# Kernel optimization log

Measured on AMD Instinct MI355X. Metric: run time of the kernel, lower is better.

## Reference

```python
import jax, jax.numpy as jnp
import numpy as np

L, H, NH, NKV, HD, FF, V = 2, 2048, 16, 2, 128, 11008, 32000
B, S, R, LORA_SCALE = 32, 64, 16, 2.0  # lora scaling = alpha/r = 32/16
PH, TD = 1024, 512
ROPE_THETA = 1e6

def _rms(x, w, eps=1e-6):
    return x * jax.lax.rsqrt(jnp.mean(x * x, axis=-1, keepdims=True) + eps) * w

def _rot_half(x):
    h = x.shape[-1] // 2
    return jnp.concatenate([-x[..., h:], x[..., :h]], axis=-1)

def _lora_linear(x, W, A, Bm, b=None):
    y = x @ W.T + LORA_SCALE * ((x @ A.T) @ Bm.T)
    return y + b if b is not None else y

def _forward(input_ids, attention_mask, embed, Wq, bq, Aq, Bq, Wk, bk, Ak, Bk,
             Wv, bv, Av, Bv, Wo, Ao, Bo, ln1, ln2, Wg, Wu, Wd, norm_f,
             W1, b1, W2, b2):
    Bsz, Sl = input_ids.shape
    h = embed[input_ids]                                            # [B,S,H]
    inv_freq = 1.0 / (ROPE_THETA ** (jnp.arange(0, HD, 2, dtype=jnp.float32) / HD))
    ang = jnp.arange(Sl, dtype=jnp.float32)[:, None] * inv_freq      # [S,HD/2]
    cos = jnp.concatenate([jnp.cos(ang)] * 2, -1)[None, :, None, :]  # [1,S,1,HD]
    sin = jnp.concatenate([jnp.sin(ang)] * 2, -1)[None, :, None, :]
    causal = jnp.tril(jnp.ones((Sl, Sl), dtype=bool))
    keep = causal[None, None] & (attention_mask[:, None, None, :] > 0)
    bias = jnp.where(keep, 0.0, -1e9).astype(jnp.float32)            # [B,1,S,S]
    for l in range(L):
        x = _rms(h, ln1[l])
        q = _lora_linear(x, Wq[l], Aq[l], Bq[l], bq[l]).reshape(Bsz, Sl, NH, HD)
        k = _lora_linear(x, Wk[l], Ak[l], Bk[l], bk[l]).reshape(Bsz, Sl, NKV, HD)
        v = _lora_linear(x, Wv[l], Av[l], Bv[l], bv[l]).reshape(Bsz, Sl, NKV, HD)
        q = q * cos + _rot_half(q) * sin
        k = k * cos + _rot_half(k) * sin
        k = jnp.repeat(k, NH // NKV, axis=2)                         # GQA expand
        v = jnp.repeat(v, NH // NKV, axis=2)
        scores = jnp.einsum('bqhd,bkhd->bhqk', q, k) / np.sqrt(HD).astype(np.float32) + bias
        p = jax.nn.softmax(scores, axis=-1)
        attn = jnp.einsum('bhqk,bkhd->bqhd', p, v).reshape(Bsz, Sl, H)
        h = h + _lora_linear(attn, Wo[l], Ao[l], Bo[l])
        x = _rms(h, ln2[l])
        h = h + (jax.nn.silu(x @ Wg[l].T) * (x @ Wu[l].T)) @ Wd[l].T  # SwiGLU MLP
    h = _rms(h, norm_f)                       # final norm -> hidden_states[-1]
    seq_len = jnp.sum(attention_mask, axis=1) - 1
    pooled = h[jnp.arange(Bsz), seq_len]      # last valid token  [B,H]
    z = jax.nn.gelu(pooled @ W1.T + b1, approximate=False)
    return (z @ W2.T + b2).astype(jnp.float32)  # [B,512]

def setup_inputs():
    key = jax.random.key(0)
    ks = jax.random.split(key, 32)
    def n(k, shape, s=0.02):
        return (s * jax.random.normal(k, shape)).astype(jnp.float32)
    lens = jax.random.randint(ks[0], (B,), 1, S + 1)
    return {
        'input_ids': jax.random.randint(ks[1], (B, S), 0, V, dtype=jnp.int32),
        'attention_mask': (jnp.arange(S)[None, :] < lens[:, None]).astype(jnp.int32),
        'embed': n(ks[2], (V, H)),
        'Wq': n(ks[3], (L, H, H)), 'bq': n(ks[4], (L, H)),
        'Aq': n(ks[5], (L, R, H)), 'Bq': n(ks[6], (L, H, R)),
        'Wk': n(ks[7], (L, NKV * HD, H)), 'bk': n(ks[8], (L, NKV * HD)),
        'Ak': n(ks[9], (L, R, H)), 'Bk': n(ks[10], (L, NKV * HD, R)),
        'Wv': n(ks[11], (L, NKV * HD, H)), 'bv': n(ks[12], (L, NKV * HD)),
        'Av': n(ks[13], (L, R, H)), 'Bv': n(ks[14], (L, NKV * HD, R)),
        'Wo': n(ks[15], (L, H, H)),
        'Ao': n(ks[16], (L, R, H)), 'Bo': n(ks[17], (L, H, R)),
        'ln1': jnp.ones((L, H), jnp.float32), 'ln2': jnp.ones((L, H), jnp.float32),
        'Wg': n(ks[18], (L, FF, H)), 'Wu': n(ks[19], (L, FF, H)), 'Wd': n(ks[20], (L, H, FF)),
        'norm_f': jnp.ones((H,), jnp.float32),
        'W1': n(ks[21], (PH, H)), 'b1': jnp.zeros((PH,), jnp.float32),
        'W2': n(ks[22], (TD, PH)), 'b2': jnp.zeros((TD,), jnp.float32),
    }

def reference(input_ids, attention_mask, embed, Wq, bq, Aq, Bq, Wk, bk, Ak, Bk,
              Wv, bv, Av, Bv, Wo, Ao, Bo, ln1, ln2, Wg, Wu, Wd, norm_f,
              W1, b1, W2, b2):
    return _forward(input_ids, attention_mask, embed, Wq, bq, Aq, Bq, Wk, bk, Ak, Bk,
                    Wv, bv, Av, Bv, Wo, Ao, Bo, ln1, ln2, Wg, Wu, Wd, norm_f,
                    W1, b1, W2, b2)
```

## Files before the change

kernel.cpp:

```cpp
#include <hip/hip_runtime.h>
#include <hip/hip_bf16.h>
#include <math.h>

namespace {
constexpr int NL  = 2;
constexpr int H   = 2048;
constexpr int NH  = 16;
constexpr int NKV = 2;
constexpr int HD  = 128;
constexpr int FF  = 11008;
constexpr int BB  = 32;
constexpr int SS  = 64;
constexpr int RR  = 16;
constexpr int TT  = BB * SS;
constexpr int KVD = NKV * HD;
constexpr int QKVD = H + 2 * KVD;
constexpr int PH  = 1024, TDm = 512;
constexpr float LSCALE = 2.0f;
}

typedef __bf16 bf16x8 __attribute__((ext_vector_type(8)));
typedef float  f32x4  __attribute__((ext_vector_type(4)));

__device__ __forceinline__ ushort4 f4_to_bf4(float4 r) {
  __hip_bfloat16 a = __float2bfloat16(r.x), b = __float2bfloat16(r.y),
                 c = __float2bfloat16(r.z), d = __float2bfloat16(r.w);
  return make_ushort4(*(unsigned short*)&a, *(unsigned short*)&b,
                      *(unsigned short*)&c, *(unsigned short*)&d);
}

__device__ __forceinline__ bf16x8 f8cvt(float4 a, float4 b) {
  bf16x8 r;
  r[0] = (__bf16)a.x; r[1] = (__bf16)a.y; r[2] = (__bf16)a.z; r[3] = (__bf16)a.w;
  r[4] = (__bf16)b.x; r[5] = (__bf16)b.y; r[6] = (__bf16)b.z; r[7] = (__bf16)b.w;
  return r;
}

__device__ __forceinline__ float dot4(float4 a, float4 b) {
  return a.x * b.x + a.y * b.y + a.z * b.z + a.w * b.w;
}

__global__ __launch_bounds__(256) void k_embed(const int* __restrict__ ids,
                                               const float* __restrict__ emb,
                                               float* __restrict__ h) {
  int t = blockIdx.x;
  long id = ids[t];
  const float4* src = reinterpret_cast<const float4*>(emb + id * (long)H);
  float4* dst = reinterpret_cast<float4*>(h + (long)t * H);
  for (int i = threadIdx.x; i < H / 4; i += 256) dst[i] = src[i];
}

__global__ __launch_bounds__(256) void k_cvt(const float* __restrict__ src,
                                             __hip_bfloat16* __restrict__ dst, long n) {
  long i = ((long)blockIdx.x * 256 + threadIdx.x) * 4;
  if (i >= n) return;
  float4 v = *reinterpret_cast<const float4*>(src + i);
  *reinterpret_cast<ushort4*>(dst + i) = f4_to_bf4(v);
}

__global__ __launch_bounds__(256) void k_cvt_qkv(
    const float* __restrict__ Wq, const float* __restrict__ Wk,
    const float* __restrict__ Wv, __hip_bfloat16* __restrict__ dst) {
  long i = ((long)blockIdx.x * 256 + threadIdx.x) * 4;
  const long n1 = (long)H * H, n2 = n1 + (long)KVD * H, nt = (long)QKVD * H;
  if (i >= nt) return;
  const float* src; long off;
  if (i < n1)      { src = Wq; off = i; }
  else if (i < n2) { src = Wk; off = i - n1; }
  else             { src = Wv; off = i - n2; }
  float4 v = *reinterpret_cast<const float4*>(src + off);
  *reinterpret_cast<ushort4*>(dst + i) = f4_to_bf4(v);
}

__global__ __launch_bounds__(256) void k_cvt3(
    const float* __restrict__ s0, const float* __restrict__ s1,
    const float* __restrict__ s2, __hip_bfloat16* __restrict__ dst) {
  long i = ((long)blockIdx.x * 256 + threadIdx.x) * 4;
  const long n = (long)FF * H;
  if (i >= 3 * n) return;
  const float* src; long off;
  if (i < n)          { src = s0; off = i; }
  else if (i < 2 * n) { src = s1; off = i - n; }
  else                { src = s2; off = i - 2 * n; }
  float4 v = *reinterpret_cast<const float4*>(src + off);
  *reinterpret_cast<ushort4*>(dst + i) = f4_to_bf4(v);
}

__global__ __launch_bounds__(256) void k_prep(
    const float* __restrict__ bq, const float* __restrict__ bk, const float* __restrict__ bv,
    const float* __restrict__ Bq, const float* __restrict__ Bk, const float* __restrict__ Bv,
    float* __restrict__ biascat, float* __restrict__ bcat) {
  int idx = blockIdx.x * 256 + threadIdx.x;
  if (idx >= NL * QKVD) return;
  int l = idx / QKVD, col = idx % QKVD;
  const float* bsrc; const float* Bsrc;
  if (col < H)            { bsrc = bq + (long)l * H + col;            Bsrc = Bq + ((long)l * H + col) * RR; }
  else if (col < H + KVD) { bsrc = bk + (long)l * KVD + (col - H);    Bsrc = Bk + ((long)l * KVD + col - H) * RR; }
  else                    { bsrc = bv + (long)l * KVD + (col - H - KVD); Bsrc = Bv + ((long)l * KVD + col - H - KVD) * RR; }
  biascat[idx] = *bsrc;
  #pragma unroll
  for (int r = 0; r < RR; ++r) bcat[(long)idx * RR + r] = Bsrc[r];
}

__global__ __launch_bounds__(256) void k_rmsnorm(const float* __restrict__ in,
                                                 const float* __restrict__ w,
                                                 float* __restrict__ out,
                                                 __hip_bfloat16* __restrict__ outb) {
  int t = blockIdx.x, tid = threadIdx.x;
  const float4* xr = reinterpret_cast<const float4*>(in + (long)t * H);
  float4 v0 = xr[tid], v1 = xr[tid + 256];
  float ss = v0.x*v0.x + v0.y*v0.y + v0.z*v0.z + v0.w*v0.w
           + v1.x*v1.x + v1.y*v1.y + v1.z*v1.z + v1.w*v1.w;
  #pragma unroll
  for (int off = 32; off; off >>= 1) ss += __shfl_xor(ss, off);
  __shared__ float sred[4];
  if ((tid & 63) == 0) sred[tid >> 6] = ss;
  __syncthreads();
  float scale = rsqrtf((sred[0] + sred[1] + sred[2] + sred[3]) * (1.0f / H) + 1e-6f);
  const float4* wr = reinterpret_cast<const float4*>(w);
  float4 w0 = wr[tid], w1 = wr[tid + 256];
  float4 r0 = make_float4(v0.x*scale*w0.x, v0.y*scale*w0.y, v0.z*scale*w0.z, v0.w*scale*w0.w);
  float4 r1 = make_float4(v1.x*scale*w1.x, v1.y*scale*w1.y, v1.z*scale*w1.z, v1.w*scale*w1.w);
  float4* o = reinterpret_cast<float4*>(out + (long)t * H);
  o[tid] = r0; o[tid + 256] = r1;
  ushort4* ob = reinterpret_cast<ushort4*>(outb + (long)t * H);
  ob[tid] = f4_to_bf4(r0); ob[tid + 256] = f4_to_bf4(r1);
}

enum { ME_BIAS_F32 = 0, ME_ACC_F32 = 1 };

__device__ __forceinline__ int raster_sw(int bid, int nwg) {
  int q8 = nwg >> 3, r8 = nwg & 7;
  int xcd = bid & 7, pos = bid >> 3;
  return (xcd < r8 ? xcd * (q8 + 1) : r8 * (q8 + 1) + (xcd - r8) * q8) + pos;
}

template <int EPI, bool LORA, bool WBF16>
__global__ __launch_bounds__(256, 3) void k_mgemm(
    const __hip_bfloat16* __restrict__ Abf,
    const float* __restrict__ W0, const float* __restrict__ W1, const float* __restrict__ W2,
    const __hip_bfloat16* __restrict__ Wb,
    const float* __restrict__ bias,
    float* __restrict__ Cf,
    const float* __restrict__ lt, const float* __restrict__ lB, int ltStride,
    int qkvMode, int M, int N, int K) {
  constexpr int BM = 64, BN = 128, BK = 64;
  constexpr int FM = 4, FN = 2;
  __shared__ __align__(16) __bf16 As[2][BM * BK];
  __shared__ __align__(16) __bf16 Bs[2][BN * BK];
  const int tid = threadIdx.x;
  const int sw = raster_sw(blockIdx.x, gridDim.x);
  const int ntm = M / BM;
  const int bm = (sw % ntm) * BM, bn = (sw / ntm) * BN;
  const int lane = tid & 63, wv = tid >> 6;
  const int wn = wv * 32;
  const int lr15 = lane & 15;
  const int g4 = lane >> 4;
  f32x4 acc[FM][FN] = {};
  const __bf16* Ag = reinterpret_cast<const __bf16*>(Abf) + (long)bm * K;

  const float* Wsrc = W0; int wrow0 = bn;
  if constexpr (!WBF16) {
    if (qkvMode) {
      if (bn >= H + KVD)      { Wsrc = W2; wrow0 = bn - (H + KVD); }
      else if (bn >= H)       { Wsrc = W1; wrow0 = bn - H; }
    }
  }
  const __bf16* Wg16 = reinterpret_cast<const __bf16*>(Wb) + (long)bn * K;

  const int arow = tid >> 3, acol = tid & 7;

  auto stageA = [&](int buf, int k0) {
    __builtin_amdgcn_global_load_lds(
        (const __attribute__((address_space(1))) void*)
          (Ag + (long)arow * K + k0 + ((acol ^ (arow & 7)) << 3)),
        (__attribute__((address_space(3))) void*)(&As[buf][tid * 8]), 16, 0, 0);
    int r1 = arow + 32;
    __builtin_amdgcn_global_load_lds(
        (const __attribute__((address_space(1))) void*)
          (Ag + (long)r1 * K + k0 + ((acol ^ (r1 & 7)) << 3)),
        (__attribute__((address_space(3))) void*)(&As[buf][(tid + 256) * 8]), 16, 0, 0);
  };

  auto stageB16 = [&](int buf, int k0) {
    #pragma unroll
    for (int q = 0; q < 4; ++q) {
      int c = tid + q * 256;
      int row = c >> 3, col = c & 7;
      __builtin_amdgcn_global_load_lds(
          (const __attribute__((address_space(1))) void*)
            (Wg16 + (long)row * K + k0 + ((col ^ (row & 7)) << 3)),
          (__attribute__((address_space(3))) void*)(&Bs[buf][c * 8]), 16, 0, 0);
    }
  };

  float4 bb[4][2];
  auto loadB = [&](int k0) {
    #pragma unroll
    for (int q = 0; q < 4; ++q) {
      int r = arow + q * 32;
      const float* p = Wsrc + (long)(wrow0 + r) * K + k0 + ((acol ^ (r & 7)) << 3);
      bb[q][0] = *reinterpret_cast<const float4*>(p);
      bb[q][1] = *reinterpret_cast<const float4*>(p + 4);
    }
  };
  auto writeB = [&](int buf) {
    #pragma unroll
    for (int q = 0; q < 4; ++q)
      *reinterpret_cast<bf16x8*>(&Bs[buf][(tid + q * 256) * 8]) = f8cvt(bb[q][0], bb[q][1]);
  };

  auto compute = [&](int buf) {
    #pragma unroll
    for (int ks = 0; ks < 2; ++ks) {
      bf16x8 af[FM], bfr[FN];
      #pragma unroll
      for (int m = 0; m < FM; ++m) {
        int row = m * 16 + lr15;
        af[m] = *reinterpret_cast<const bf16x8*>(
            &As[buf][row * BK + (((g4 + 4 * ks) ^ (row & 7)) << 3)]);
      }
      #pragma unroll
      for (int n = 0; n < FN; ++n) {
        int row = wn + n * 16 + lr15;
        bfr[n] = *reinterpret_cast<const bf16x8*>(
            &Bs[buf][row * BK + (((g4 + 4 * ks) ^ (row & 7)) << 3)]);
      }
      #pragma unroll
      for (int m = 0; m < FM; ++m)
        #pragma unroll
        for (int n = 0; n < FN; ++n)
          acc[m][n] = __builtin_amdgcn_mfma_f32_16x16x32_bf16(af[m], bfr[n], acc[m][n], 0, 0, 0);
    }
  };

  const int NS = K / BK;
  if constexpr (WBF16) {
    stageA(0, 0); stageB16(0, 0);
    __syncthreads();
    int cur = 0;
    for (int t = 0; t < NS; ++t) {
      if (t + 1 < NS) { stageA(cur ^ 1, (t + 1) * BK); stageB16(cur ^ 1, (t + 1) * BK); }
      compute(cur);
      if (t + 1 < NS) { __syncthreads(); cur ^= 1; }
    }
  } else {
    loadB(0);
    stageA(0, 0);
    writeB(0);
    __syncthreads();
    int cur = 0;
    for (int t = 0; t < NS; ++t) {
      if (t + 1 < NS) { loadB((t + 1) * BK); stageA(cur ^ 1, (t + 1) * BK); }
      compute(cur);
      if (t + 1 < NS) {
        writeB(cur ^ 1);
        __syncthreads();
        cur ^= 1;
      }
    }
  }

  const int r0 = g4 << 2;
  float4 lb[FN][4];
  int goff = 0;
  if constexpr (LORA) {
    if (qkvMode) goff = (bn >= H + KVD) ? 32 : (bn >= H ? 16 : 0);
    #pragma unroll
    for (int n = 0; n < FN; ++n) {
      const float4* p = reinterpret_cast<const float4*>(lB + (long)(bn + wn + n * 16 + lr15) * RR);
      lb[n][0] = p[0]; lb[n][1] = p[1]; lb[n][2] = p[2]; lb[n][3] = p[3];
    }
  }
  float bcol[FN];
  if constexpr (EPI == ME_BIAS_F32) {
    #pragma unroll
    for (int n = 0; n < FN; ++n) bcol[n] = bias[bn + wn + n * 16 + lr15];
  }
  #pragma unroll
  for (int m = 0; m < FM; ++m)
    #pragma unroll
    for (int j = 0; j < 4; ++j) {
      const long row = bm + m * 16 + r0 + j;
      float lv[FN];
      if constexpr (LORA) {
        const float4* tp = reinterpret_cast<const float4*>(lt + row * ltStride + goff);
        float4 t0 = tp[0], t1 = tp[1], t2 = tp[2], t3 = tp[3];
        #pragma unroll
        for (int n = 0; n < FN; ++n)
          lv[n] = LSCALE * (dot4(t0, lb[n][0]) + dot4(t1, lb[n][1]) +
                            dot4(t2, lb[n][2]) + dot4(t3, lb[n][3]));
      }
      #pragma unroll
      for (int n = 0; n < FN; ++n) {
        const int col = bn + wn + n * 16 + lr15;
        float v = acc[m][n][j];
        if constexpr (LORA) v += lv[n];
        if constexpr (EPI == ME_BIAS_F32) Cf[row * N + col] = v + bcol[n];
        else                              Cf[row * N + col] += v;
      }
    }
}

__global__ __launch_bounds__(256, 2) void k_swiglu_b(
    const __hip_bfloat16* __restrict__ Abf,
    const __hip_bfloat16* __restrict__ Wgb,
    const __hip_bfloat16* __restrict__ Wub,
    __hip_bfloat16* __restrict__ Cb,
    int M, int N, int K) {
  constexpr int BM = 128, BN = 128, BK = 32;
  constexpr int FM = 4, FN = 4;
  constexpr int ACH = BM * BK / 8;
  __shared__ __align__(16) __bf16 As[2][BM * BK];
  __shared__ __align__(16) __bf16 Gs[2][BN * BK];
  __shared__ __align__(16) __bf16 Us[2][BN * BK];
  const int tid = threadIdx.x;
  const int sw = raster_sw(blockIdx.x, gridDim.x);
  const int ntm = M / BM;
  const int bm = (sw % ntm) * BM, bn = (sw / ntm) * BN;
  const int lane = tid & 63, wv = tid >> 6;
  const int wm = (wv >> 1) * 64, wn = (wv & 1) * 64;
  const int lr15 = lane & 15;
  const int lks = (((lane >> 4) << 3)) ^ ((((lr15 >> 1) & 3)) << 3);
  f32x4 accg[FM][FN] = {}, accu[FM][FN] = {};
  const __bf16* Ag = reinterpret_cast<const __bf16*>(Abf) + (long)bm * K;
  const __bf16* Gg = reinterpret_cast<const __bf16*>(Wgb) + (long)bn * K;
  const __bf16* Ug = reinterpret_cast<const __bf16*>(Wub) + (long)bn * K;

  auto stage = [&](int buf, int k0) {
    #pragma unroll
    for (int i = tid; i < ACH; i += 256) {
      const int sc = ((i & 3) ^ ((i >> 3) & 3)) << 3;
      const long ro = (long)(i >> 2) * K + k0 + sc;
      __builtin_amdgcn_global_load_lds(
          (const __attribute__((address_space(1))) void*)(Ag + ro),
          (__attribute__((address_space(3))) void*)(&As[buf][i * 8]), 16, 0, 0);
      __builtin_amdgcn_global_load_lds(
          (const __attribute__((address_space(1))) void*)(Gg + ro),
          (__attribute__((address_space(3))) void*)(&Gs[buf][i * 8]), 16, 0, 0);
      __builtin_amdgcn_global_load_lds(
          (const __attribute__((address_space(1))) void*)(Ug + ro),
          (__attribute__((address_space(3))) void*)(&Us[buf][i * 8]), 16, 0, 0);
    }
  };
  auto compute = [&](int buf) {
    bf16x8 af[FM], gf[FN], uf[FN];
    #pragma unroll
    for (int m = 0; m < FM; ++m)
      af[m] = *reinterpret_cast<const bf16x8*>(&As[buf][(wm + m * 16 + lr15) * BK + lks]);
    #pragma unroll
    for (int n = 0; n < FN; ++n) {
      gf[n] = *reinterpret_cast<const bf16x8*>(&Gs[buf][(wn + n * 16 + lr15) * BK + lks]);
      uf[n] = *reinterpret_cast<const bf16x8*>(&Us[buf][(wn + n * 16 + lr15) * BK + lks]);
    }
    #pragma unroll
    for (int m = 0; m < FM; ++m)
      #pragma unroll
      for (int n = 0; n < FN; ++n) {
        accg[m][n] = __builtin_amdgcn_mfma_f32_16x16x32_bf16(af[m], gf[n], accg[m][n], 0, 0, 0);
        accu[m][n] = __builtin_amdgcn_mfma_f32_16x16x32_bf16(af[m], uf[n], accu[m][n], 0, 0, 0);
      }
  };

  const int NS = K / BK;
  stage(0, 0);
  asm volatile("s_waitcnt vmcnt(0)" ::: "memory");
  __builtin_amdgcn_s_barrier();
  int cur = 0;
  for (int t = 0; t < NS; ++t) {
    if (t + 1 < NS) stage(cur ^ 1, (t + 1) * BK);
    compute(cur);
    if (t + 1 < NS) {
      asm volatile("s_waitcnt vmcnt(0)" ::: "memory");
      __builtin_amdgcn_s_barrier();
      cur ^= 1;
    }
  }

  const int r0 = (lane >> 4) << 2;
  #pragma unroll
  for (int m = 0; m < FM; ++m)
    #pragma unroll
    for (int n = 0; n < FN; ++n) {
      const int col = bn + wn + n * 16 + lr15;
      const long rowb = bm + wm + m * 16 + r0;
      #pragma unroll
      for (int j = 0; j < 4; ++j) {
        float g = accg[m][n][j], u = accu[m][n][j];
        Cb[(rowb + j) * N + col] = __float2bfloat16((g / (1.0f + expf(-g))) * u);
      }
    }
}

__global__ __launch_bounds__(256, 2) void k_swiglu(
    const __hip_bfloat16* __restrict__ Abf,
    const float* __restrict__ Wg,
    const float* __restrict__ Wu,
    __hip_bfloat16* __restrict__ Cb,
    int M, int N, int K) {
  constexpr int BM = 128, BN = 128, BK = 32;
  constexpr int FM = 4, FN = 4;
  __shared__ __align__(16) __bf16 As[2][BM * BK];
  __shared__ __align__(16) __bf16 Gs[2][BN * BK];
  __shared__ __align__(16) __bf16 Us[2][BN * BK];
  const int tid = threadIdx.x;
  const int sw = raster_sw(blockIdx.x, gridDim.x);
  const int ntm = M / BM;
  const int bm = (sw % ntm) * BM, bn = (sw / ntm) * BN;
  const int lane = tid & 63, wv = tid >> 6;
  const int wm = (wv >> 1) * 64, wn = (wv & 1) * 64;
  const int lr15 = lane & 15;
  const int lks = (((lane >> 4) << 3)) ^ ((((lr15 >> 1) & 3)) << 3);
  f32x4 accg[FM][FN] = {}, accu[FM][FN] = {};
  const __bf16* Ag = reinterpret_cast<const __bf16*>(Abf) + (long)bm * K;

  const int br0 = tid >> 2, bc = tid & 3;
  const int br1 = br0 + 64;
  const float* gp0 = Wg + (long)(bn + br0) * K + bc * 8;
  const float* gp1 = Wg + (long)(bn + br1) * K + bc * 8;
  const float* up0 = Wu + (long)(bn + br0) * K + bc * 8;
  const float* up1 = Wu + (long)(bn + br1) * K + bc * 8;
  const int d0 = br0 * BK + ((bc ^ ((br0 >> 1) & 3)) << 3);
  const int d1 = br1 * BK + ((bc ^ ((br1 >> 1) & 3)) << 3);

  float4 g00, g01, g10, g11, u00, u01, u10, u11;
  auto loadB = [&](int k0) {
    g00 = *reinterpret_cast<const float4*>(gp0 + k0);
    g01 = *reinterpret_cast<const float4*>(gp0 + k0 + 4);
    g10 = *reinterpret_cast<const float4*>(gp1 + k0);
    g11 = *reinterpret_cast<const float4*>(gp1 + k0 + 4);
    u00 = *reinterpret_cast<const float4*>(up0 + k0);
    u01 = *reinterpret_cast<const float4*>(up0 + k0 + 4);
    u10 = *reinterpret_cast<const float4*>(up1 + k0);
    u11 = *reinterpret_cast<const float4*>(up1 + k0 + 4);
  };
  auto writeB = [&](int buf) {
    *reinterpret_cast<bf16x8*>(&Gs[buf][d0]) = f8cvt(g00, g01);
    *reinterpret_cast<bf16x8*>(&Gs[buf][d1]) = f8cvt(g10, g11);
    *reinterpret_cast<bf16x8*>(&Us[buf][d0]) = f8cvt(u00, u01);
    *reinterpret_cast<bf16x8*>(&Us[buf][d1]) = f8cvt(u10, u11);
  };
  auto stageA = [&](int buf, int k0) {
    #pragma unroll
    for (int i = tid; i < BM * BK / 8; i += 256)
      __builtin_amdgcn_global_load_lds(
          (const __attribute__((address_space(1))) void*)
            (Ag + (long)(i >> 2) * K + k0 + (((i & 3) ^ ((i >> 3) & 3)) << 3)),
          (__attribute__((address_space(3))) void*)(&As[buf][i * 8]), 16, 0, 0);
  };
  auto compute = [&](int buf) {
    bf16x8 af[FM], gf[FN], uf[FN];
    #pragma unroll
    for (int m = 0; m < FM; ++m)
      af[m] = *reinterpret_cast<const bf16x8*>(&As[buf][(wm + m * 16 + lr15) * BK + lks]);
    #pragma unroll
    for (int n = 0; n < FN; ++n) {
      gf[n] = *reinterpret_cast<const bf16x8*>(&Gs[buf][(wn + n * 16 + lr15) * BK + lks]);
      uf[n] = *reinterpret_cast<const bf16x8*>(&Us[buf][(wn + n * 16 + lr15) * BK + lks]);
    }
    #pragma unroll
    for (int m = 0; m < FM; ++m)
      #pragma unroll
      for (int n = 0; n < FN; ++n) {
        accg[m][n] = __builtin_amdgcn_mfma_f32_16x16x32_bf16(af[m], gf[n], accg[m][n], 0, 0, 0);
        accu[m][n] = __builtin_amdgcn_mfma_f32_16x16x32_bf16(af[m], uf[n], accu[m][n], 0, 0, 0);
      }
  };

  const int NS = K / BK;
  loadB(0);
  stageA(0, 0);
  writeB(0);
  __syncthreads();
  int cur = 0;
  for (int t = 0; t < NS; ++t) {
    if (t + 1 < NS) { loadB((t + 1) * BK); stageA(cur ^ 1, (t + 1) * BK); }
    compute(cur);
    if (t + 1 < NS) {
      writeB(cur ^ 1);
      __syncthreads();
      cur ^= 1;
    }
  }

  const int r0 = (lane >> 4) << 2;
  #pragma unroll
  for (int m = 0; m < FM; ++m)
    #pragma unroll
    for (int n = 0; n < FN; ++n) {
      const int col = bn + wn + n * 16 + lr15;
      const long rowb = bm + wm + m * 16 + r0;
      #pragma unroll
      for (int j = 0; j < 4; ++j) {
        float g = accg[m][n][j], u = accu[m][n][j];
        Cb[(rowb + j) * N + col] = __float2bfloat16((g / (1.0f + expf(-g))) * u);
      }
    }
}

template <bool GELU>
__global__ __launch_bounds__(256) void k_hgemm(const float* __restrict__ A,
                                               const float* __restrict__ W,
                                               const float* __restrict__ bias,
                                               float* __restrict__ C,
                                               int M, int N, int K) {
  int idx = blockIdx.x * 4 + (threadIdx.x >> 6);
  if (idx >= M * N) return;
  int b = idx / N, n = idx % N;
  int lane = threadIdx.x & 63;
  const float* a = A + (long)b * K;
  const float* w = W + (long)n * K;
  float s = 0.f;
  for (int k = lane * 4; k < K; k += 256) {
    float4 av = *reinterpret_cast<const float4*>(a + k);
    float4 wv = *reinterpret_cast<const float4*>(w + k);
    s = fmaf(av.x, wv.x, s); s = fmaf(av.y, wv.y, s);
    s = fmaf(av.z, wv.z, s); s = fmaf(av.w, wv.w, s);
  }
  #pragma unroll
  for (int off = 32; off; off >>= 1) s += __shfl_xor(s, off);
  if (lane == 0) {
    float v = s + bias[n];
    if (GELU) v = 0.5f * v * (1.0f + erff(v * 0.70710678118654752f));
    C[idx] = v;
  }
}

__global__ __launch_bounds__(256) void k_lora_down3(
    const float* __restrict__ x,
    const float* __restrict__ A0, const float* __restrict__ A1, const float* __restrict__ A2,
    float* __restrict__ out, int outStride) {
  int t = blockIdx.x, g = blockIdx.y, tid = threadIdx.x;
  const float* A = (g == 0) ? A0 : (g == 1) ? A1 : A2;
  int r = tid & 15, sl = tid >> 4;
  const float* xr = x + (long)t * H + sl * 128;
  const float* Ar = A + (long)r * H + sl * 128;
  float p = 0.f;
  #pragma unroll 8
  for (int kk = 0; kk < 128; kk += 4) {
    float4 xv = *reinterpret_cast<const float4*>(xr + kk);
    float4 av = *reinterpret_cast<const float4*>(Ar + kk);
    p = fmaf(xv.x, av.x, p); p = fmaf(xv.y, av.y, p);
    p = fmaf(xv.z, av.z, p); p = fmaf(xv.w, av.w, p);
  }
  __shared__ float red[16][17];
  red[sl][r] = p;
  __syncthreads();
  if (tid < 16) {
    float s = 0.f;
    #pragma unroll
    for (int i = 0; i < 16; ++i) s += red[i][tid];
    out[(long)t * outStride + g * 16 + tid] = s;
  }
}

__global__ __launch_bounds__(256) void k_rope_tab(float2* __restrict__ tab) {
  int idx = blockIdx.x * 256 + threadIdx.x;
  if (idx >= SS * 64) return;
  int pos = idx >> 6, j = idx & 63;
  float inv = 1.0f / powf(1.0e6f, (float)(2 * j) * (1.0f / HD));
  float ang = (float)pos * inv;
  tab[idx] = make_float2(cosf(ang), sinf(ang));
}

__global__ __launch_bounds__(256) void k_attn2(const float* __restrict__ qkv,
                                               const int* __restrict__ mask,
                                               const float2* __restrict__ tab,
                                               float* __restrict__ o,
                                               __hip_bfloat16* __restrict__ obf) {
  __shared__ float Kt[128][65];
  __shared__ float Vs[64][128];
  __shared__ int   mb[64];
  const int b = blockIdx.x, kv = blockIdx.y, qz = blockIdx.z;
  const int tid = threadIdx.x, lane = tid & 63, wid = tid >> 6;
  const float* kbase = qkv + ((long)b * SS) * QKVD + H + kv * HD;
  for (int i = tid; i < 64 * 64; i += 256) {
    int j = i & 63, ki = i >> 6;
    const float* kr = kbase + (long)ki * QKVD;
    float lo = kr[j], hi = kr[j + 64];
    float2 cs = tab[ki * 64 + j];
    Kt[j][ki]      = lo * cs.x - hi * cs.y;
    Kt[j + 64][ki] = hi * cs.x + lo * cs.y;
  }
  const float* vbase = qkv + ((long)b * SS) * QKVD + H + KVD + kv * HD;
  for (int i = tid; i < 64 * 32; i += 256) {
    int f4 = i & 31, ki = i >> 5;
    *reinterpret_cast<float4*>(&Vs[ki][f4 * 4]) =
        *reinterpret_cast<const float4*>(vbase + (long)ki * QKVD + f4 * 4);
  }
  if (tid < 64) mb[tid] = mask[b * SS + tid];
  __syncthreads();

  for (int rr = 0; rr < 32; ++rr) {
    int br = wid * 32 + rr;
    int qh = br >> 4, qi = qz * 16 + (br & 15);
    int hh = kv * 8 + qh;
    long t = (long)b * SS + qi;
    const float* qr = qkv + t * QKVD + hh * HD;
    float dot = 0.f;
    #pragma unroll 8
    for (int j = 0; j < 64; ++j) {
      float2 cs = tab[qi * 64 + j];
      float lo = qr[j], hi = qr[j + 64];
      float rlo = lo * cs.x - hi * cs.y;
      float rhi = hi * cs.x + lo * cs.y;
      dot = fmaf(rlo, Kt[j][lane], dot);
      dot = fmaf(rhi, Kt[j + 64][lane], dot);
    }
    bool keep = (lane <= qi) && (mb[lane] > 0);
    float sc = dot * 0.08838834764831845f + (keep ? 0.f : -1e9f);
    float m = sc;
    #pragma unroll
    for (int off = 32; off; off >>= 1) m = fmaxf(m, __shfl_xor(m, off));
    float e = expf(sc - m);
    float s = e;
    #pragma unroll
    for (int off = 32; off; off >>= 1) s += __shfl_xor(s, off);
    float p = e / s;
    float o0 = 0.f, o1 = 0.f;
    #pragma unroll 8
    for (int ki = 0; ki < 64; ++ki) {
      float pk = __shfl(p, ki);
      o0 = fmaf(pk, Vs[ki][lane], o0);
      o1 = fmaf(pk, Vs[ki][lane + 64], o1);
    }
    long oidx = t * H + hh * HD + lane;
    o[oidx] = o0; o[oidx + 64] = o1;
    obf[oidx] = __float2bfloat16(o0);
    obf[oidx + 64] = __float2bfloat16(o1);
  }
}

__global__ __launch_bounds__(256) void k_pool(const float* __restrict__ x,
                                              const int* __restrict__ mask,
                                              float* __restrict__ pooled) {
  int b = blockIdx.x;
  __shared__ int len;
  if (threadIdx.x == 0) {
    int L2 = 0;
    for (int i = 0; i < SS; ++i) L2 += (mask[b * SS + i] > 0);
    len = L2;
  }
  __syncthreads();
  const float4* sp = reinterpret_cast<const float4*>(x + ((long)b * SS + len - 1) * H);
  float4* dp = reinterpret_cast<float4*>(pooled + (long)b * H);
  for (int i = threadIdx.x; i < H / 4; i += 256) dp[i] = sp[i];
}

static inline int cvt_grid(long n) { return (int)((n / 4 + 255) / 256); }

extern "C" void kernel_launch(void* const* d_in, const int* in_sizes, int n_in,
                              void* d_out, int out_size, void* d_ws, size_t ws_size,
                              hipStream_t stream) {
  const int*   ids    = (const int*)d_in[0];
  const int*   mask   = (const int*)d_in[1];
  const float* embed  = (const float*)d_in[2];
  const float* Wq     = (const float*)d_in[3];
  const float* bq     = (const float*)d_in[4];
  const float* Aq     = (const float*)d_in[5];
  const float* Bq     = (const float*)d_in[6];
  const float* Wk     = (const float*)d_in[7];
  const float* bk     = (const float*)d_in[8];
  const float* Ak     = (const float*)d_in[9];
  const float* Bk     = (const float*)d_in[10];
  const float* Wv     = (const float*)d_in[11];
  const float* bv     = (const float*)d_in[12];
  const float* Av     = (const float*)d_in[13];
  const float* Bv     = (const float*)d_in[14];
  const float* Wo     = (const float*)d_in[15];
  const float* Ao     = (const float*)d_in[16];
  const float* Bo     = (const float*)d_in[17];
  const float* ln1    = (const float*)d_in[18];
  const float* ln2    = (const float*)d_in[19];
  const float* Wg     = (const float*)d_in[20];
  const float* Wu     = (const float*)d_in[21];
  const float* Wd     = (const float*)d_in[22];
  const float* norm_f = (const float*)d_in[23];
  const float* W1     = (const float*)d_in[24];
  const float* b1     = (const float*)d_in[25];
  const float* W2     = (const float*)d_in[26];
  const float* b2     = (const float*)d_in[27];

  float* ws = (float*)d_ws;
  float* h        = ws;
  float* x        = h    + (long)TT * H;
  float* qkv      = x    + (long)TT * H;
  float* tmpR     = qkv  + (long)TT * QKVD;
  float* tmpO     = tmpR + (long)TT * 48;
  float* pooled   = tmpO + (long)TT * 16;
  float* zz       = pooled + (long)BB * H;
  float* biascat  = zz   + (long)BB * PH;
  float* bcat     = biascat + (long)NL * QKVD;
  float2* ropetab = (float2*)(bcat + (long)NL * QKVD * RR);
  float* endf32   = (float*)(ropetab + SS * 64);
  __hip_bfloat16* x_bf  = (__hip_bfloat16*)endf32;
  __hip_bfloat16* ffbf  = x_bf + (long)TT * H;
  __hip_bfloat16* wgbf  = ffbf + (long)TT * FF;
  __hip_bfloat16* wubf  = wgbf + (long)FF * H;
  __hip_bfloat16* wdbf  = wubf + (long)FF * H;
  __hip_bfloat16* wqbf  = wdbf + (long)FF * H;
  __hip_bfloat16* wobf  = wqbf + (long)QKVD * H;
  size_t need_bf = (size_t)((char*)(wobf + (long)H * H) - (char*)d_ws);
  bool bfw = ws_size >= need_bf;

  k_embed<<<TT, 256, 0, stream>>>(ids, embed, h);
  k_rope_tab<<<(SS * 64 + 255) / 256, 256, 0, stream>>>(ropetab);
  k_prep<<<(NL * QKVD + 255) / 256, 256, 0, stream>>>(bq, bk, bv, Bq, Bk, Bv, biascat, bcat);

  for (int l = 0; l < NL; ++l) {
    const long lHH = (long)l * H * H;
    const long lKH = (long)l * KVD * H;
    const long lRH = (long)l * RR * H;
    const long lFH = (long)l * FF * H;
    k_rmsnorm<<<TT, 256, 0, stream>>>(h, ln1 + l * H, x, x_bf);
    k_lora_down3<<<dim3(TT, 3), 256, 0, stream>>>(
        x, Aq + lRH, Ak + lRH, Av + lRH, tmpR, 48);
    if (bfw) {
      k_cvt_qkv<<<cvt_grid((long)QKVD * H), 256, 0, stream>>>(
          Wq + lHH, Wk + lKH, Wv + lKH, wqbf);
      k_mgemm<ME_BIAS_F32, true, true><<<(TT / 64) * (QKVD / 128), 256, 0, stream>>>(
          x_bf, nullptr, nullptr, nullptr, wqbf, biascat + (long)l * QKVD, qkv,
          tmpR, bcat + (long)l * QKVD * RR, 48, 1, TT, QKVD, H);
    } else {
      k_mgemm<ME_BIAS_F32, true, false><<<(TT / 64) * (QKVD / 128), 256, 0, stream>>>(
          x_bf, Wq + lHH, Wk + lKH, Wv + lKH, nullptr, biascat + (long)l * QKVD, qkv,
          tmpR, bcat + (long)l * QKVD * RR, 48, 1, TT, QKVD, H);
    }
    k_attn2<<<dim3(BB, NKV, 4), 256, 0, stream>>>(qkv, mask, ropetab, x, x_bf);
    k_lora_down3<<<dim3(TT, 1), 256, 0, stream>>>(
        x, Ao + lRH, Ao + lRH, Ao + lRH, tmpO, 16);
    if (bfw) {
      k_cvt<<<cvt_grid((long)H * H), 256, 0, stream>>>(Wo + lHH, wobf, (long)H * H);
      k_mgemm<ME_ACC_F32, true, true><<<(TT / 64) * (H / 128), 256, 0, stream>>>(
          x_bf, nullptr, nullptr, nullptr, wobf, nullptr, h,
          tmpO, Bo + (long)l * H * RR, 16, 0, TT, H, H);
    } else {
      k_mgemm<ME_ACC_F32, true, false><<<(TT / 64) * (H / 128), 256, 0, stream>>>(
          x_bf, Wo + lHH, Wo + lHH, Wo + lHH, nullptr, nullptr, h,
          tmpO, Bo + (long)l * H * RR, 16, 0, TT, H, H);
    }
    k_rmsnorm<<<TT, 256, 0, stream>>>(h, ln2 + l * H, x, x_bf);
    if (bfw) {
      k_cvt3<<<cvt_grid(3L * FF * H), 256, 0, stream>>>(
          Wg + lFH, Wu + lFH, Wd + lFH, wgbf);
      k_swiglu_b<<<(TT / 128) * (FF / 128), 256, 0, stream>>>(
          x_bf, wgbf, wubf, ffbf, TT, FF, H);
      k_mgemm<ME_ACC_F32, false, true><<<(TT / 64) * (H / 128), 256, 0, stream>>>(
          ffbf, nullptr, nullptr, nullptr, wdbf, nullptr, h,
          nullptr, nullptr, 0, 0, TT, H, FF);
    } else {
      k_swiglu<<<(TT / 128) * (FF / 128), 256, 0, stream>>>(
          x_bf, Wg + lFH, Wu + lFH, ffbf, TT, FF, H);
      k_mgemm<ME_ACC_F32, false, false><<<(TT / 64) * (H / 128), 256, 0, stream>>>(
          ffbf, Wd + lFH, Wd + lFH, Wd + lFH, nullptr, nullptr, h,
          nullptr, nullptr, 0, 0, TT, H, FF);
    }
  }

  k_rmsnorm<<<TT, 256, 0, stream>>>(h, norm_f, x, x_bf);
  k_pool<<<BB, 256, 0, stream>>>(x, mask, pooled);
  k_hgemm<true><<<(BB * PH + 3) / 4, 256, 0, stream>>>(pooled, W1, b1, zz, BB, PH, H);
  k_hgemm<false><<<(BB * TDm + 3) / 4, 256, 0, stream>>>(zz, W2, b2, (float*)d_out, BB, TDm, PH);
}
```

Measured before the change: 1.874 ms.

## Retile bf16 SwiGLU GEMM to 64x128x64 with XOR-swizzled LDS layout

```diff
diff --git a/kernel.cpp b/kernel.cpp
--- a/kernel.cpp
+++ b/kernel.cpp
@@ -308,9 +308,8 @@
     const __hip_bfloat16* __restrict__ Wub,
     __hip_bfloat16* __restrict__ Cb,
     int M, int N, int K) {
-  constexpr int BM = 128, BN = 128, BK = 32;
-  constexpr int FM = 4, FN = 4;
-  constexpr int ACH = BM * BK / 8;
+  constexpr int BM = 64, BN = 128, BK = 64;
+  constexpr int FM = 4, FN = 2;
   __shared__ __align__(16) __bf16 As[2][BM * BK];
   __shared__ __align__(16) __bf16 Gs[2][BN * BK];
   __shared__ __align__(16) __bf16 Us[2][BN * BK];
@@ -319,71 +318,86 @@
   const int ntm = M / BM;
   const int bm = (sw % ntm) * BM, bn = (sw / ntm) * BN;
   const int lane = tid & 63, wv = tid >> 6;
-  const int wm = (wv >> 1) * 64, wn = (wv & 1) * 64;
+  const int wn = wv * 32;
   const int lr15 = lane & 15;
-  const int lks = (((lane >> 4) << 3)) ^ ((((lr15 >> 1) & 3)) << 3);
+  const int g4 = lane >> 4;
   f32x4 accg[FM][FN] = {}, accu[FM][FN] = {};
   const __bf16* Ag = reinterpret_cast<const __bf16*>(Abf) + (long)bm * K;
   const __bf16* Gg = reinterpret_cast<const __bf16*>(Wgb) + (long)bn * K;
   const __bf16* Ug = reinterpret_cast<const __bf16*>(Wub) + (long)bn * K;
 
+  const int arow = tid >> 3, acol = tid & 7;
+
   auto stage = [&](int buf, int k0) {
-    #pragma unroll
-    for (int i = tid; i < ACH; i += 256) {
-      const int sc = ((i & 3) ^ ((i >> 3) & 3)) << 3;
-      const long ro = (long)(i >> 2) * K + k0 + sc;
-      __builtin_amdgcn_global_load_lds(
-          (const __attribute__((address_space(1))) void*)(Ag + ro),
-          (__attribute__((address_space(3))) void*)(&As[buf][i * 8]), 16, 0, 0);
+    __builtin_amdgcn_global_load_lds(
+        (const __attribute__((address_space(1))) void*)
+          (Ag + (long)arow * K + k0 + ((acol ^ (arow & 7)) << 3)),
+        (__attribute__((address_space(3))) void*)(&As[buf][tid * 8]), 16, 0, 0);
+    int r1 = arow + 32;
+    __builtin_amdgcn_global_load_lds(
+        (const __attribute__((address_space(1))) void*)
+          (Ag + (long)r1 * K + k0 + ((acol ^ (r1 & 7)) << 3)),
+        (__attribute__((address_space(3))) void*)(&As[buf][(tid + 256) * 8]), 16, 0, 0);
+    #pragma unroll
+    for (int q = 0; q < 4; ++q) {
+      int c = tid + q * 256;
+      int row = c >> 3, col = c & 7;
+      const long ro = (long)row * K + k0 + ((col ^ (row & 7)) << 3);
       __builtin_amdgcn_global_load_lds(
           (const __attribute__((address_space(1))) void*)(Gg + ro),
-          (__attribute__((address_space(3))) void*)(&Gs[buf][i * 8]), 16, 0, 0);
+          (__attribute__((address_space(3))) void*)(&Gs[buf][c * 8]), 16, 0, 0);
       __builtin_amdgcn_global_load_lds(
           (const __attribute__((address_space(1))) void*)(Ug + ro),
-          (__attribute__((address_space(3))) void*)(&Us[buf][i * 8]), 16, 0, 0);
+          (__attribute__((address_space(3))) void*)(&Us[buf][c * 8]), 16, 0, 0);
     }
   };
   auto compute = [&](int buf) {
-    bf16x8 af[FM], gf[FN], uf[FN];
-    #pragma unroll
-    for (int m = 0; m < FM; ++m)
-      af[m] = *reinterpret_cast<const bf16x8*>(&As[buf][(wm + m * 16 + lr15) * BK + lks]);
-    #pragma unroll
-    for (int n = 0; n < FN; ++n) {
-      gf[n] = *reinterpret_cast<const bf16x8*>(&Gs[buf][(wn + n * 16 + lr15) * BK + lks]);
-      uf[n] = *reinterpret_cast<const bf16x8*>(&Us[buf][(wn + n * 16 + lr15) * BK + lks]);
-    }
-    #pragma unroll
-    for (int m = 0; m < FM; ++m)
+    #pragma unroll
+    for (int ks = 0; ks < 2; ++ks) {
+      bf16x8 af[FM], gf[FN], uf[FN];
+      #pragma unroll
+      for (int m = 0; m < FM; ++m) {
+        int row = m * 16 + lr15;
+        af[m] = *reinterpret_cast<const bf16x8*>(
+            &As[buf][row * BK + (((g4 + 4 * ks) ^ (row & 7)) << 3)]);
+      }
       #pragma unroll
       for (int n = 0; n < FN; ++n) {
-        accg[m][n] = __builtin_amdgcn_mfma_f32_16x16x32_bf16(af[m], gf[n], accg[m][n], 0, 0, 0);
-        accu[m][n] = __builtin_amdgcn_mfma_f32_16x16x32_bf16(af[m], uf[n], accu[m][n], 0, 0, 0);
-      }
+        int row = wn + n * 16 + lr15;
+        const int off = row * BK + (((g4 + 4 * ks) ^ (row & 7)) << 3);
+        gf[n] = *reinterpret_cast<const bf16x8*>(&Gs[buf][off]);
+        uf[n] = *reinterpret_cast<const bf16x8*>(&Us[buf][off]);
+      }
+      #pragma unroll
+      for (int m = 0; m < FM; ++m)
+        #pragma unroll
+        for (int n = 0; n < FN; ++n) {
+          accg[m][n] = __builtin_amdgcn_mfma_f32_16x16x32_bf16(af[m], gf[n], accg[m][n], 0, 0, 0);
+          accu[m][n] = __builtin_amdgcn_mfma_f32_16x16x32_bf16(af[m], uf[n], accu[m][n], 0, 0, 0);
+        }
+    }
   };
 
   const int NS = K / BK;
   stage(0, 0);
-  asm volatile("s_waitcnt vmcnt(0)" ::: "memory");
-  __builtin_amdgcn_s_barrier();
+  __syncthreads();
   int cur = 0;
   for (int t = 0; t < NS; ++t) {
     if (t + 1 < NS) stage(cur ^ 1, (t + 1) * BK);
     compute(cur);
     if (t + 1 < NS) {
-      asm volatile("s_waitcnt vmcnt(0)" ::: "memory");
-      __builtin_amdgcn_s_barrier();
+      __syncthreads();
       cur ^= 1;
     }
   }
 
-  const int r0 = (lane >> 4) << 2;
+  const int r0 = g4 << 2;
   #pragma unroll
   for (int m = 0; m < FM; ++m)
     #pragma unroll
     for (int n = 0; n < FN; ++n) {
       const int col = bn + wn + n * 16 + lr15;
-      const long rowb = bm + wm + m * 16 + r0;
+      const long rowb = bm + m * 16 + r0;
       #pragma unroll
       for (int j = 0; j < 4; ++j) {
         float g = accg[m][n][j], u = accu[m][n][j];
@@ -743,7 +757,7 @@
     if (bfw) {
       k_cvt3<<<cvt_grid(3L * FF * H), 256, 0, stream>>>(
           Wg + lFH, Wu + lFH, Wd + lFH, wgbf);
-      k_swiglu_b<<<(TT / 128) * (FF / 128), 256, 0, stream>>>(
+      k_swiglu_b<<<(TT / 64) * (FF / 128), 256, 0, stream>>>(
           x_bf, wgbf, wubf, ffbf, TT, FF, H);
       k_mgemm<ME_ACC_F32, false, true><<<(TT / 64) * (H / 128), 256, 0, stream>>>(
           ffbf, nullptr, nullptr, nullptr, wdbf, nullptr, h,
```

Measured after the change: 1.951 ms. 1.04x slower.
